# Optimization experiments

Measured on AMD Instinct MI355X. Metric: run time of the kernel, lower is better.

Reference implementation:

```python
import jax, jax.numpy as jnp
import numpy as np

B, S, D, H, DK = 2, 2048, 1024, 16, 64  # d_model = n_heads * d_k

def setup_inputs() -> dict:
    key = jax.random.key(0)
    ks = jax.random.split(key, 11)
    s = 1.0 / np.sqrt(D)
    return {
        "Q": jax.random.normal(ks[0], (B, S, D), jnp.float32),
        "K": jax.random.normal(ks[1], (B, S, D), jnp.float32),
        "V": jax.random.normal(ks[2], (B, S, D), jnp.float32),
        "wq": jax.random.normal(ks[3], (D, D), jnp.float32) * s,
        "bq": jnp.zeros((D,), jnp.float32),
        "wk": jax.random.normal(ks[4], (D, D), jnp.float32) * s,
        "bk": jnp.zeros((D,), jnp.float32),
        "wv": jax.random.normal(ks[5], (D, D), jnp.float32) * s,
        "bv": jnp.zeros((D,), jnp.float32),
        "wo": jax.random.normal(ks[6], (D, D), jnp.float32) * s,
        "bo": jnp.zeros((D,), jnp.float32),
    }

def reference(Q, K, V, wq, bq, wk, bk, wv, bv, wo, bo):
    # linear projections (torch Linear: x @ W^T + b)
    q = Q @ wq.T + bq
    k = K @ wk.T + bk
    v = V @ wv.T + bv
    # split heads -> [B, H, S, DK]
    def split(t):
        return t.reshape(B, S, H, DK).transpose(0, 2, 1, 3)
    q, k, v = split(q), split(k), split(v)
    scale = 1.0 / np.sqrt(DK)
    scores = jnp.einsum('bhqd,bhkd->bhqk', q, k) * scale  # [B,H,S,S]
    probs = jax.nn.softmax(scores, axis=-1)
    # dropout is identity in eval mode
    ctx = jnp.einsum('bhqk,bhkd->bhqd', probs, v)  # [B,H,S,DK]
    ctx = ctx.transpose(0, 2, 1, 3).reshape(B, S, D)
    return ctx @ wo.T + bo
```

## Files before the change

### kernel.cpp

```cpp
#include <hip/hip_runtime.h>

#define S_LEN 2048
#define DMODEL 1024
#define DHEAD 64

typedef _Float16 half8 __attribute__((ext_vector_type(8)));
typedef _Float16 half4 __attribute__((ext_vector_type(4)));
typedef float f32x4 __attribute__((ext_vector_type(4)));
typedef int i32x4 __attribute__((ext_vector_type(4)));

#define LOG2E 1.4426950408889634f

__device__ __forceinline__ void async_copy16(const void* g, void* l) {
  __builtin_amdgcn_global_load_lds((__attribute__((address_space(1))) const void*)g,
                                   (__attribute__((address_space(3))) void*)l,
                                   16, 0, 0);
}

#define WAIT_VMCNT(N) asm volatile("s_waitcnt vmcnt(" #N ")" ::: "memory")
#define WAIT_LGKM0() asm volatile("s_waitcnt lgkmcnt(0)" ::: "memory")
#define RAW_BARRIER() asm volatile("s_barrier" ::: "memory")

__global__ __launch_bounds__(256) void convert_w(const float* __restrict__ wq,
                                                 const float* __restrict__ wk,
                                                 const float* __restrict__ wv,
                                                 _Float16* __restrict__ dst) {
  const float* src = (blockIdx.y == 0) ? wq : (blockIdx.y == 1) ? wk : wv;
  _Float16* d = dst + (size_t)blockIdx.y * (DMODEL * DMODEL);
  int i = (blockIdx.x * 256 + threadIdx.x) * 4;
  float4 v = *(const float4*)(src + i);
  half4 h;
  h[0] = (_Float16)v.x; h[1] = (_Float16)v.y;
  h[2] = (_Float16)v.z; h[3] = (_Float16)v.w;
  *(half4*)(d + i) = h;
}

__global__ __launch_bounds__(256) void convert_wo(const float* __restrict__ wo,
                                                  _Float16* __restrict__ dst) {
  int i = (blockIdx.x * 256 + threadIdx.x) * 4;
  float4 v = *(const float4*)(wo + i);
  half4 h;
  h[0] = (_Float16)v.x; h[1] = (_Float16)v.y;
  h[2] = (_Float16)v.z; h[3] = (_Float16)v.w;
  *(half4*)(dst + i) = h;
}

__global__ __launch_bounds__(256, 3) void qkv_gemm(
    const float* __restrict__ Qf, const float* __restrict__ Kf, const float* __restrict__ Vf,
    const _Float16* __restrict__ wh,
    const float* __restrict__ bq, const float* __restrict__ bk, const float* __restrict__ bv,
    _Float16* __restrict__ qo, _Float16* __restrict__ ko, _Float16* __restrict__ vt) {
  __shared__ __align__(16) _Float16 Asb[3][128 * 32];
  __shared__ __align__(16) _Float16 Bsb[3][128 * 32];
  const int tid = threadIdx.x;
  const int wave = tid >> 6, lane = tid & 63;
  const int m15 = lane & 15, quad = lane >> 4;
  const int m0 = blockIdx.x * 128;
  const int y = blockIdx.y;
  const int sel = (y < 8) ? 2 : (y < 16) ? 0 : 1;
  const int n0 = (y & 7) * 128;
  const float* Ag = (sel == 0) ? Qf : (sel == 1) ? Kf : Vf;
  const _Float16* Wg = wh + (size_t)sel * (DMODEL * DMODEL);
  const float* bias = (sel == 0) ? bq : (sel == 1) ? bk : bv;

  const int wm = (wave & 1) * 64, wn = (wave >> 1) * 64;

  const int sr = tid >> 1, sc16 = (tid & 1) * 16;
  const int g0 = (tid & 1) * 2, asw = (sr >> 1) & 3;
  const int b_r = lane >> 2, b_g = (lane & 3) ^ ((lane >> 3) & 3);
  const int ra = ((quad ^ ((m15 >> 1) & 3)) << 4);

  f32x4 acc[4][4];
#pragma unroll
  for (int i = 0; i < 4; i++)
#pragma unroll
    for (int j = 0; j < 4; j++) {
      f32x4 z = {0.f, 0.f, 0.f, 0.f};
      acc[i][j] = z;
    }

  const float* ap = Ag + (size_t)(m0 + sr) * DMODEL + sc16;

  auto loadA = [&](int kk, float4 (&s)[4]) {
    const float* p = ap + kk;
    s[0] = ((const float4*)p)[0];
    s[1] = ((const float4*)p)[1];
    s[2] = ((const float4*)p)[2];
    s[3] = ((const float4*)p)[3];
  };
  auto writeA = [&](const float4 (&s)[4], int nb) {
    half8 h0, h1;
    h0[0] = (_Float16)s[0].x; h0[1] = (_Float16)s[0].y; h0[2] = (_Float16)s[0].z; h0[3] = (_Float16)s[0].w;
    h0[4] = (_Float16)s[1].x; h0[5] = (_Float16)s[1].y; h0[6] = (_Float16)s[1].z; h0[7] = (_Float16)s[1].w;
    h1[0] = (_Float16)s[2].x; h1[1] = (_Float16)s[2].y; h1[2] = (_Float16)s[2].z; h1[3] = (_Float16)s[2].w;
    h1[4] = (_Float16)s[3].x; h1[5] = (_Float16)s[3].y; h1[6] = (_Float16)s[3].z; h1[7] = (_Float16)s[3].w;
    char* rb = (char*)&Asb[nb][0] + sr * 64;
    *(half8*)(rb + ((g0 ^ asw) << 4)) = h0;
    *(half8*)(rb + (((g0 + 1) ^ asw) << 4)) = h1;
  };
  auto issueB = [&](int kk, int nb) {
#pragma unroll
    for (int p = 0; p < 2; p++) {
      int row = (p * 4 + wave) * 16 + b_r;
      async_copy16(Wg + (size_t)(n0 + row) * DMODEL + kk + b_g * 8,
                   (char*)&Bsb[nb][0] + p * 4096 + wave * 1024);
    }
  };
  auto compute = [&](int m3) {
    const char* ab = (const char*)&Asb[m3][0];
    const char* bb = (const char*)&Bsb[m3][0];
    half8 af[4], bf[4];
#pragma unroll
    for (int i = 0; i < 4; i++)
      af[i] = *(const half8*)(ab + (wm + i * 16 + m15) * 64 + ra);
#pragma unroll
    for (int j = 0; j < 4; j++)
      bf[j] = *(const half8*)(bb + (wn + j * 16 + m15) * 64 + ra);
#pragma unroll
    for (int i = 0; i < 4; i++)
#pragma unroll
      for (int j = 0; j < 4; j++)
        acc[i][j] = __builtin_amdgcn_mfma_f32_16x16x32_f16(af[i], bf[j], acc[i][j], 0, 0, 0);
  };

  float4 s0[4], s1[4], s2[4];

  issueB(0, 0);
  loadA(0, s0);
  issueB(32, 1);
  loadA(32, s1);
  loadA(64, s2);
  WAIT_VMCNT(10);
  writeA(s0, 0);
  WAIT_LGKM0();
  RAW_BARRIER();

  auto body = [&](int kt, int m3, int bB, int bW, float4 (&ld)[4], const float4 (&wr)[4],
                  int mode) {
    if (mode == 0) {
      issueB((kt + 2) * 32, bB);
      loadA((kt + 3) * 32, ld);
    } else if (mode == 1) {
      issueB((kt + 2) * 32, bB);
    }
    compute(m3);
    if (mode == 3) return;
    if (mode == 0) { WAIT_VMCNT(10); }
    else if (mode == 1) { WAIT_VMCNT(6); }
    else { WAIT_VMCNT(0); }
    writeA(wr, bW);
    WAIT_LGKM0();
    RAW_BARRIER();
  };

#pragma unroll 1
  for (int k3 = 0; k3 < 27; k3 += 3) {
    body(k3 + 0, 0, 2, 1, s0, s1, 0);
    body(k3 + 1, 1, 0, 2, s1, s2, 0);
    body(k3 + 2, 2, 1, 0, s2, s0, 0);
  }
  body(27, 0, 2, 1, s0, s1, 0);
  body(28, 1, 0, 2, s1, s2, 0);
  body(29, 2, 1, 0, s2, s0, 1);
  body(30, 0, 0, 1, s0, s1, 2);
  body(31, 1, 0, 0, s0, s0, 3);

  if (sel != 2) {
    _Float16* outp = (sel == 0) ? qo : ko;
    const float scale = (sel == 0) ? (0.125f * LOG2E) : 1.0f;
#pragma unroll
    for (int i = 0; i < 4; i++) {
#pragma unroll
      for (int j = 0; j < 4; j++) {
        int gn = n0 + wn + j * 16 + m15;
        float bb = bias[gn];
#pragma unroll
        for (int r = 0; r < 4; r++) {
          int gm = m0 + wm + i * 16 + quad * 4 + r;
          outp[(size_t)gm * DMODEL + gn] = (_Float16)((acc[i][j][r] + bb) * scale);
        }
      }
    }
  } else {
#pragma unroll
    for (int i = 0; i < 4; i++) {
      int gm0 = m0 + wm + i * 16 + quad * 4;
      int b = gm0 >> 11, s = gm0 & 2047;
#pragma unroll
      for (int j = 0; j < 4; j++) {
        int gn = n0 + wn + j * 16 + m15;
        int h = gn >> 6, dk = gn & 63;
        float bb = bias[gn];
        half4 hv;
        hv[0] = (_Float16)(acc[i][j][0] + bb);
        hv[1] = (_Float16)(acc[i][j][1] + bb);
        hv[2] = (_Float16)(acc[i][j][2] + bb);
        hv[3] = (_Float16)(acc[i][j][3] + bb);
        *(half4*)(vt + ((size_t)(b * 16 + h) * 64 + dk) * 2048 + s) = hv;
      }
    }
  }
}

__global__ __launch_bounds__(256) void attn_kernel(const _Float16* __restrict__ qh,
                                                   const _Float16* __restrict__ kh,
                                                   const _Float16* __restrict__ vt,
                                                   _Float16* __restrict__ ctx) {
  __shared__ __align__(16) char smem[49152];
  const int tid = threadIdx.x;
  const int wave = tid >> 6, lane = tid & 63;
  const int m15 = lane & 15, qd = lane >> 4;
  const int wq = wave >> 1, ws = wave & 1;
  const int q0 = blockIdx.x * 64;
  const int h = blockIdx.y, b = blockIdx.z;
  const size_t base = (size_t)b * S_LEN * DMODEL + (size_t)h * DHEAD;
  const size_t vbase = (size_t)(b * 16 + h) * 64 * 2048;

  half8 qf[2][2];
#pragma unroll
  for (int qt = 0; qt < 2; qt++) {
    const _Float16* qp = qh + base + (size_t)(q0 + wq * 32 + qt * 16 + m15) * DMODEL + qd * 8;
    qf[qt][0] = *(const half8*)qp;
    qf[qt][1] = *(const half8*)(qp + 32);
  }

  const int l8 = lane >> 3, s8 = lane & 7;
  const int swz = (s8 ^ l8) * 8;
  const _Float16* ksrc = kh + base + (size_t)(wave * 8 + l8) * DMODEL + swz;
  const _Float16* vsrc = vt + vbase + (size_t)(wave * 8 + l8) * S_LEN + swz;

  const int kgr = ((qd ^ (m15 & 7)) << 4);
  const int vgr = (((ws * 4 + qd) ^ (m15 & 7)) << 4);
  const int krow = ws * 32 + m15;

  auto stage = [&](int tile, int bufi) {
    const int kv = tile * 64;
    char* kd = smem + bufi * 8192 + wave * 1024;
    char* vd = smem + 24576 + bufi * 8192 + wave * 1024;
#pragma unroll
    for (int p = 0; p < 2; p++) {
      async_copy16(ksrc + (size_t)(kv + p * 32) * DMODEL, kd + p * 4096);
      async_copy16(vsrc + (size_t)(p * 32) * S_LEN + kv, vd + p * 4096);
    }
  };

  f32x4 acc[4][2];
#pragma unroll
  for (int i = 0; i < 4; i++)
#pragma unroll
    for (int j = 0; j < 2; j++) { f32x4 z = {0.f, 0.f, 0.f, 0.f}; acc[i][j] = z; }
  float ls[2] = {0.f, 0.f};

  stage(0, 0);
  stage(1, 1);
  WAIT_VMCNT(4);
  RAW_BARRIER();

  int bcur = 0, bnxt = 2;
  for (int it = 0; it < 32; it++) {
    if (it < 30) stage(it + 2, bnxt);
    const char* kb = smem + bcur * 8192;
    const char* vb = smem + 24576 + bcur * 8192;

    half8 kf[2][2];
#pragma unroll
    for (int t = 0; t < 2; t++) {
      kf[t][0] = *(const half8*)(kb + (krow + 16 * t) * 128 + kgr);
      kf[t][1] = *(const half8*)(kb + (krow + 16 * t) * 128 + (kgr ^ 64));
    }

    f32x4 sc[2][2];
#pragma unroll
    for (int t = 0; t < 2; t++)
#pragma unroll
      for (int qt = 0; qt < 2; qt++) {
        f32x4 z = {0.f, 0.f, 0.f, 0.f};
        sc[t][qt] = __builtin_amdgcn_mfma_f32_16x16x32_f16(kf[t][0], qf[qt][0], z, 0, 0, 0);
        sc[t][qt] = __builtin_amdgcn_mfma_f32_16x16x32_f16(kf[t][1], qf[qt][1], sc[t][qt], 0, 0, 0);
      }

    int pk[2][2][2];
#pragma unroll
    for (int t = 0; t < 2; t++)
#pragma unroll
      for (int qt = 0; qt < 2; qt++) {
        float e0 = __builtin_amdgcn_exp2f(sc[t][qt][0]);
        float e1 = __builtin_amdgcn_exp2f(sc[t][qt][1]);
        float e2 = __builtin_amdgcn_exp2f(sc[t][qt][2]);
        float e3 = __builtin_amdgcn_exp2f(sc[t][qt][3]);
        ls[qt] += (e0 + e1) + (e2 + e3);
        pk[t][qt][0] = __builtin_bit_cast(int, __builtin_amdgcn_cvt_pkrtz(e0, e1));
        pk[t][qt][1] = __builtin_bit_cast(int, __builtin_amdgcn_cvt_pkrtz(e2, e3));
      }

    half8 pA[2];
#pragma unroll
    for (int qt = 0; qt < 2; qt++) {
      i32x4 fh;
#pragma unroll
      for (int p = 0; p < 2; p++) {
        auto s1 = __builtin_amdgcn_permlane32_swap(pk[0][qt][p], pk[1][qt][p], false, false);
        auto s2 = __builtin_amdgcn_permlane16_swap(s1[0], s1[1], false, false);
        fh[p] = (int)s2[0];
        fh[2 + p] = (int)s2[1];
      }
      pA[qt] = __builtin_bit_cast(half8, fh);
    }

#pragma unroll
    for (int td = 0; td < 4; td++) {
      half8 vf = *(const half8*)(vb + (td * 16 + m15) * 128 + vgr);
#pragma unroll
      for (int qt = 0; qt < 2; qt++)
        acc[td][qt] = __builtin_amdgcn_mfma_f32_16x16x32_f16(vf, pA[qt], acc[td][qt], 0, 0, 0);
    }
    if (it < 30) { WAIT_VMCNT(4); } else { WAIT_VMCNT(0); }
    RAW_BARRIER();
    bcur = (bcur == 2) ? 0 : bcur + 1;
    bnxt = (bnxt == 2) ? 0 : bnxt + 1;
  }

  float* Ored = (float*)smem;
  float* Lred = (float*)(smem + 17408);

#pragma unroll
  for (int qt = 0; qt < 2; qt++) {
    ls[qt] += __shfl_xor(ls[qt], 16);
    ls[qt] += __shfl_xor(ls[qt], 32);
  }

  if (ws == 1) {
#pragma unroll
    for (int qt = 0; qt < 2; qt++) {
      int q = wq * 32 + qt * 16 + m15;
      if (qd == 0) Lred[q] = ls[qt];
#pragma unroll
      for (int td = 0; td < 4; td++)
        *(f32x4*)&Ored[q * 68 + td * 16 + qd * 4] = acc[td][qt];
    }
  }
  __syncthreads();

  if (ws == 0) {
#pragma unroll
    for (int qt = 0; qt < 2; qt++) {
      int q = wq * 32 + qt * 16 + m15;
      const float inv = 1.0f / (ls[qt] + Lred[q]);
#pragma unroll
      for (int td = 0; td < 4; td++) {
        f32x4 o = acc[td][qt] + *(const f32x4*)&Ored[q * 68 + td * 16 + qd * 4];
        half4 hv;
#pragma unroll
        for (int r = 0; r < 4; r++) hv[r] = (_Float16)(o[r] * inv);
        *(half4*)(ctx + base + (size_t)(q0 + q) * DMODEL + td * 16 + qd * 4) = hv;
      }
    }
  }
}

__global__ __launch_bounds__(256, 4) void out_gemm(const _Float16* __restrict__ ch,
                                                   const _Float16* __restrict__ who,
                                                   const float* __restrict__ bo,
                                                   float* __restrict__ out) {
  __shared__ __align__(16) _Float16 As[3][64 * 32];
  __shared__ __align__(16) _Float16 Bs[3][128 * 32];
  const int tid = threadIdx.x;
  const int wave = tid >> 6, lane = tid & 63;
  const int m15 = lane & 15, quad = lane >> 4;
  const int m0 = blockIdx.x * 64, n0 = blockIdx.y * 128;
  const int wm = (wave & 1) * 32, wn = (wave >> 1) * 64;
  const int b_r = lane >> 2, b_g = (lane & 3) ^ ((lane >> 3) & 3);
  const int rgr = ((quad ^ ((m15 >> 1) & 3)) << 4);

  f32x4 acc[2][4];
#pragma unroll
  for (int i = 0; i < 2; i++)
#pragma unroll
    for (int j = 0; j < 4; j++) {
      f32x4 z = {0.f, 0.f, 0.f, 0.f};
      acc[i][j] = z;
    }

  auto issueTile = [&](int kk, int nb) {
    {
      int row = wave * 16 + b_r;
      async_copy16(ch + (size_t)(m0 + row) * DMODEL + kk + b_g * 8,
                   (char*)&As[nb][0] + wave * 1024);
    }
#pragma unroll
    for (int p = 0; p < 2; p++) {
      int row = (p * 4 + wave) * 16 + b_r;
      async_copy16(who + (size_t)(n0 + row) * DMODEL + kk + b_g * 8,
                   (char*)&Bs[nb][0] + p * 4096 + wave * 1024);
    }
  };
  auto compute = [&](int m3) {
    half8 af[2], bf[4];
#pragma unroll
    for (int i = 0; i < 2; i++)
      af[i] = *(const half8*)((char*)&As[m3][0] + (wm + i * 16 + m15) * 64 + rgr);
#pragma unroll
    for (int j = 0; j < 4; j++)
      bf[j] = *(const half8*)((char*)&Bs[m3][0] + (wn + j * 16 + m15) * 64 + rgr);
#pragma unroll
    for (int i = 0; i < 2; i++)
#pragma unroll
      for (int j = 0; j < 4; j++)
        acc[i][j] = __builtin_amdgcn_mfma_f32_16x16x32_f16(af[i], bf[j], acc[i][j], 0, 0, 0);
  };

  issueTile(0, 0);
  issueTile(32, 1);
  WAIT_VMCNT(3);
  RAW_BARRIER();

#pragma unroll 1
  for (int k3 = 0; k3 < 30; k3 += 3) {
    issueTile((k3 + 2) * 32, 2); compute(0); WAIT_VMCNT(3); RAW_BARRIER();
    issueTile((k3 + 3) * 32, 0); compute(1); WAIT_VMCNT(3); RAW_BARRIER();
    issueTile((k3 + 4) * 32, 1); compute(2); WAIT_VMCNT(3); RAW_BARRIER();
  }
  compute(0);
  WAIT_VMCNT(0);
  RAW_BARRIER();
  compute(1);

#pragma unroll
  for (int i = 0; i < 2; i++) {
#pragma unroll
    for (int j = 0; j < 4; j++) {
      int gn = n0 + wn + j * 16 + m15;
      float bb = bo[gn];
#pragma unroll
      for (int r = 0; r < 4; r++) {
        int gm = m0 + wm + i * 16 + quad * 4 + r;
        out[(size_t)gm * DMODEL + gn] = acc[i][j][r] + bb;
      }
    }
  }
}

extern "C" void kernel_launch(void* const* d_in, const int* in_sizes, int n_in,
                              void* d_out, int out_size, void* d_ws, size_t ws_size,
                              hipStream_t stream) {
  (void)in_sizes; (void)n_in; (void)out_size; (void)ws_size;
  const float* Q  = (const float*)d_in[0];
  const float* K  = (const float*)d_in[1];
  const float* V  = (const float*)d_in[2];
  const float* wq = (const float*)d_in[3];
  const float* bq = (const float*)d_in[4];
  const float* wk = (const float*)d_in[5];
  const float* bk = (const float*)d_in[6];
  const float* wv = (const float*)d_in[7];
  const float* bv = (const float*)d_in[8];
  const float* wo = (const float*)d_in[9];
  const float* bo = (const float*)d_in[10];
  float* out = (float*)d_out;

  _Float16* qh = (_Float16*)d_out;
  _Float16* kh = qh + (size_t)4194304;
  _Float16* vt = (_Float16*)d_ws;
  _Float16* wh = vt + (size_t)4194304;
  _Float16* ch = vt + (size_t)4194304;
  _Float16* who = (_Float16*)d_ws;

  convert_w<<<dim3(1024, 3), 256, 0, stream>>>(wq, wk, wv, wh);
  qkv_gemm<<<dim3(32, 24), 256, 0, stream>>>(Q, K, V, wh, bq, bk, bv, qh, kh, vt);
  attn_kernel<<<dim3(32, 16, 2), 256, 0, stream>>>(qh, kh, vt, ch);
  convert_wo<<<dim3(1024), 256, 0, stream>>>(wo, who);
  out_gemm<<<dim3(64, 8), 256, 0, stream>>>(ch, who, bo, out);
}
```

Measured before the change: 232.0 us.

## Load V fragments directly from global in attention, restructure output GEMM tiling

The attention kernel stops staging V through LDS and reads the V^T fragments straight from global memory into registers each iteration. K staging drops from triple to double buffering, with __syncthreads replacing the explicit vmcnt waits, and the reduction scratch padding shrinks so total LDS is about 16KB instead of 48KB, which may raise occupancy. The output GEMM moves to 64x64 tiles with a 64-wide K step and double buffering, doubling the grid. The risk is that uncoalesced, unshared V global loads now sit in the critical path of each iteration, and the full barrier may serialize the K prefetch.

```diff
diff --git a/kernel.cpp b/kernel.cpp
--- a/kernel.cpp
+++ b/kernel.cpp
@@ -206,7 +206,7 @@
                                                    const _Float16* __restrict__ kh,
                                                    const _Float16* __restrict__ vt,
                                                    _Float16* __restrict__ ctx) {
-  __shared__ __align__(16) char smem[49152];
+  __shared__ __align__(16) char smem[16640];
   const int tid = threadIdx.x;
   const int wave = tid >> 6, lane = tid & 63;
   const int m15 = lane & 15, qd = lane >> 4;
@@ -227,22 +227,11 @@
   const int l8 = lane >> 3, s8 = lane & 7;
   const int swz = (s8 ^ l8) * 8;
   const _Float16* ksrc = kh + base + (size_t)(wave * 8 + l8) * DMODEL + swz;
-  const _Float16* vsrc = vt + vbase + (size_t)(wave * 8 + l8) * S_LEN + swz;
+  char* kdst = smem + wave * 1024;
 
   const int kgr = ((qd ^ (m15 & 7)) << 4);
-  const int vgr = (((ws * 4 + qd) ^ (m15 & 7)) << 4);
   const int krow = ws * 32 + m15;
-
-  auto stage = [&](int tile, int bufi) {
-    const int kv = tile * 64;
-    char* kd = smem + bufi * 8192 + wave * 1024;
-    char* vd = smem + 24576 + bufi * 8192 + wave * 1024;
-#pragma unroll
-    for (int p = 0; p < 2; p++) {
-      async_copy16(ksrc + (size_t)(kv + p * 32) * DMODEL, kd + p * 4096);
-      async_copy16(vsrc + (size_t)(p * 32) * S_LEN + kv, vd + p * 4096);
-    }
-  };
+  const _Float16* vrow = vt + vbase + (size_t)m15 * 2048 + ws * 32 + qd * 8;
 
   f32x4 acc[4][2];
 #pragma unroll
@@ -251,16 +240,21 @@
     for (int j = 0; j < 2; j++) { f32x4 z = {0.f, 0.f, 0.f, 0.f}; acc[i][j] = z; }
   float ls[2] = {0.f, 0.f};
 
-  stage(0, 0);
-  stage(1, 1);
-  WAIT_VMCNT(4);
-  RAW_BARRIER();
-
-  int bcur = 0, bnxt = 2;
+#pragma unroll
+  for (int p = 0; p < 2; p++)
+    async_copy16(ksrc + (size_t)(p * 32) * DMODEL, kdst + p * 4096);
+  __syncthreads();
+
   for (int it = 0; it < 32; it++) {
-    if (it < 30) stage(it + 2, bnxt);
-    const char* kb = smem + bcur * 8192;
-    const char* vb = smem + 24576 + bcur * 8192;
+    const int buf = it & 1;
+    if (it < 31) {
+      const int kv = (it + 1) * 64;
+#pragma unroll
+      for (int p = 0; p < 2; p++)
+        async_copy16(ksrc + (size_t)(kv + p * 32) * DMODEL, kdst + (buf ^ 1) * 8192 + p * 4096);
+    }
+    const char* kb = smem + buf * 8192;
+    const int kv0 = it * 64;
 
     half8 kf[2][2];
 #pragma unroll
@@ -278,6 +272,11 @@
         sc[t][qt] = __builtin_amdgcn_mfma_f32_16x16x32_f16(kf[t][0], qf[qt][0], z, 0, 0, 0);
         sc[t][qt] = __builtin_amdgcn_mfma_f32_16x16x32_f16(kf[t][1], qf[qt][1], sc[t][qt], 0, 0, 0);
       }
+
+    half8 vf0 = *(const half8*)(vrow + kv0);
+    half8 vf1 = *(const half8*)(vrow + 16 * 2048 + kv0);
+    half8 vf2 = *(const half8*)(vrow + 32 * 2048 + kv0);
+    half8 vf3 = *(const half8*)(vrow + 48 * 2048 + kv0);
 
     int pk[2][2][2];
 #pragma unroll
@@ -308,20 +307,17 @@
     }
 
 #pragma unroll
-    for (int td = 0; td < 4; td++) {
-      half8 vf = *(const half8*)(vb + (td * 16 + m15) * 128 + vgr);
-#pragma unroll
-      for (int qt = 0; qt < 2; qt++)
-        acc[td][qt] = __builtin_amdgcn_mfma_f32_16x16x32_f16(vf, pA[qt], acc[td][qt], 0, 0, 0);
-    }
-    if (it < 30) { WAIT_VMCNT(4); } else { WAIT_VMCNT(0); }
-    RAW_BARRIER();
-    bcur = (bcur == 2) ? 0 : bcur + 1;
-    bnxt = (bnxt == 2) ? 0 : bnxt + 1;
+    for (int qt = 0; qt < 2; qt++) {
+      acc[0][qt] = __builtin_amdgcn_mfma_f32_16x16x32_f16(vf0, pA[qt], acc[0][qt], 0, 0, 0);
+      acc[1][qt] = __builtin_amdgcn_mfma_f32_16x16x32_f16(vf1, pA[qt], acc[1][qt], 0, 0, 0);
+      acc[2][qt] = __builtin_amdgcn_mfma_f32_16x16x32_f16(vf2, pA[qt], acc[2][qt], 0, 0, 0);
+      acc[3][qt] = __builtin_amdgcn_mfma_f32_16x16x32_f16(vf3, pA[qt], acc[3][qt], 0, 0, 0);
+    }
+    __syncthreads();
   }
 
   float* Ored = (float*)smem;
-  float* Lred = (float*)(smem + 17408);
+  float* Lred = (float*)(smem + 16384);
 
 #pragma unroll
   for (int qt = 0; qt < 2; qt++) {
@@ -336,7 +332,7 @@
       if (qd == 0) Lred[q] = ls[qt];
 #pragma unroll
       for (int td = 0; td < 4; td++)
-        *(f32x4*)&Ored[q * 68 + td * 16 + qd * 4] = acc[td][qt];
+        *(f32x4*)&Ored[q * 64 + td * 16 + qd * 4] = acc[td][qt];
     }
   }
   __syncthreads();
@@ -348,7 +344,7 @@
       const float inv = 1.0f / (ls[qt] + Lred[q]);
 #pragma unroll
       for (int td = 0; td < 4; td++) {
-        f32x4 o = acc[td][qt] + *(const f32x4*)&Ored[q * 68 + td * 16 + qd * 4];
+        f32x4 o = acc[td][qt] + *(const f32x4*)&Ored[q * 64 + td * 16 + qd * 4];
         half4 hv;
 #pragma unroll
         for (int r = 0; r < 4; r++) hv[r] = (_Float16)(o[r] * inv);
@@ -358,77 +354,76 @@
   }
 }
 
-__global__ __launch_bounds__(256, 4) void out_gemm(const _Float16* __restrict__ ch,
-                                                   const _Float16* __restrict__ who,
-                                                   const float* __restrict__ bo,
-                                                   float* __restrict__ out) {
-  __shared__ __align__(16) _Float16 As[3][64 * 32];
-  __shared__ __align__(16) _Float16 Bs[3][128 * 32];
+__global__ __launch_bounds__(256) void out_gemm(const _Float16* __restrict__ ch,
+                                                const _Float16* __restrict__ who,
+                                                const float* __restrict__ bo,
+                                                float* __restrict__ out) {
+  __shared__ __align__(16) _Float16 As[2][64 * 64];
+  __shared__ __align__(16) _Float16 Bs[2][64 * 64];
   const int tid = threadIdx.x;
   const int wave = tid >> 6, lane = tid & 63;
   const int m15 = lane & 15, quad = lane >> 4;
-  const int m0 = blockIdx.x * 64, n0 = blockIdx.y * 128;
-  const int wm = (wave & 1) * 32, wn = (wave >> 1) * 64;
-  const int b_r = lane >> 2, b_g = (lane & 3) ^ ((lane >> 3) & 3);
-  const int rgr = ((quad ^ ((m15 >> 1) & 3)) << 4);
-
-  f32x4 acc[2][4];
+  const int m0 = blockIdx.x * 64, n0 = blockIdx.y * 64;
+  const int wm = (wave & 1) * 32, wn = (wave >> 1) * 32;
+
+  const int l8 = lane >> 3, s8 = lane & 7;
+  const int swz = (s8 ^ l8) * 8;
+  const _Float16* asrc = ch + (size_t)(m0 + wave * 8 + l8) * DMODEL + swz;
+  const _Float16* bsrc = who + (size_t)(n0 + wave * 8 + l8) * DMODEL + swz;
+  char* adst = (char*)&As[0][0] + wave * 1024;
+  char* bdst = (char*)&Bs[0][0] + wave * 1024;
+
+  const int rg0 = ((quad ^ (m15 & 7)) << 4);
+
+  f32x4 acc[2][2];
 #pragma unroll
   for (int i = 0; i < 2; i++)
 #pragma unroll
-    for (int j = 0; j < 4; j++) {
+    for (int j = 0; j < 2; j++) {
       f32x4 z = {0.f, 0.f, 0.f, 0.f};
       acc[i][j] = z;
     }
 
-  auto issueTile = [&](int kk, int nb) {
-    {
-      int row = wave * 16 + b_r;
-      async_copy16(ch + (size_t)(m0 + row) * DMODEL + kk + b_g * 8,
-                   (char*)&As[nb][0] + wave * 1024);
-    }
+  auto stage = [&](int kk, int bufi) {
 #pragma unroll
     for (int p = 0; p < 2; p++) {
-      int row = (p * 4 + wave) * 16 + b_r;
-      async_copy16(who + (size_t)(n0 + row) * DMODEL + kk + b_g * 8,
-                   (char*)&Bs[nb][0] + p * 4096 + wave * 1024);
-    }
-  };
-  auto compute = [&](int m3) {
-    half8 af[2], bf[4];
+      async_copy16(asrc + (size_t)(p * 32) * DMODEL + kk, adst + bufi * 8192 + p * 4096);
+      async_copy16(bsrc + (size_t)(p * 32) * DMODEL + kk, bdst + bufi * 8192 + p * 4096);
+    }
+  };
+
+  stage(0, 0);
+  __syncthreads();
+
+  for (int kt = 0; kt < 16; kt++) {
+    const int buf = kt & 1;
+    if (kt < 15) stage((kt + 1) * 64, buf ^ 1);
+    const char* ab = (const char*)&As[buf][0];
+    const char* bb = (const char*)&Bs[buf][0];
+    half8 af[2][2], bf[2][2];
+#pragma unroll
+    for (int i = 0; i < 2; i++) {
+      af[i][0] = *(const half8*)(ab + (wm + i * 16 + m15) * 128 + rg0);
+      af[i][1] = *(const half8*)(ab + (wm + i * 16 + m15) * 128 + (rg0 ^ 64));
+    }
+#pragma unroll
+    for (int j = 0; j < 2; j++) {
+      bf[j][0] = *(const half8*)(bb + (wn + j * 16 + m15) * 128 + rg0);
+      bf[j][1] = *(const half8*)(bb + (wn + j * 16 + m15) * 128 + (rg0 ^ 64));
+    }
 #pragma unroll
     for (int i = 0; i < 2; i++)
-      af[i] = *(const half8*)((char*)&As[m3][0] + (wm + i * 16 + m15) * 64 + rgr);
-#pragma unroll
-    for (int j = 0; j < 4; j++)
-      bf[j] = *(const half8*)((char*)&Bs[m3][0] + (wn + j * 16 + m15) * 64 + rgr);
-#pragma unroll
-    for (int i = 0; i < 2; i++)
-#pragma unroll
-      for (int j = 0; j < 4; j++)
-        acc[i][j] = __builtin_amdgcn_mfma_f32_16x16x32_f16(af[i], bf[j], acc[i][j], 0, 0, 0);
-  };
-
-  issueTile(0, 0);
-  issueTile(32, 1);
-  WAIT_VMCNT(3);
-  RAW_BARRIER();
-
-#pragma unroll 1
-  for (int k3 = 0; k3 < 30; k3 += 3) {
-    issueTile((k3 + 2) * 32, 2); compute(0); WAIT_VMCNT(3); RAW_BARRIER();
-    issueTile((k3 + 3) * 32, 0); compute(1); WAIT_VMCNT(3); RAW_BARRIER();
-    issueTile((k3 + 4) * 32, 1); compute(2); WAIT_VMCNT(3); RAW_BARRIER();
-  }
-  compute(0);
-  WAIT_VMCNT(0);
-  RAW_BARRIER();
-  compute(1);
-
+#pragma unroll
+      for (int j = 0; j < 2; j++) {
+        acc[i][j] = __builtin_amdgcn_mfma_f32_16x16x32_f16(af[i][0], bf[j][0], acc[i][j], 0, 0, 0);
+        acc[i][j] = __builtin_amdgcn_mfma_f32_16x16x32_f16(af[i][1], bf[j][1], acc[i][j], 0, 0, 0);
+      }
+    __syncthreads();
+  }
 #pragma unroll
   for (int i = 0; i < 2; i++) {
 #pragma unroll
-    for (int j = 0; j < 4; j++) {
+    for (int j = 0; j < 2; j++) {
       int gn = n0 + wn + j * 16 + m15;
       float bb = bo[gn];
 #pragma unroll
@@ -468,5 +463,5 @@
   qkv_gemm<<<dim3(32, 24), 256, 0, stream>>>(Q, K, V, wh, bq, bk, bv, qh, kh, vt);
   attn_kernel<<<dim3(32, 16, 2), 256, 0, stream>>>(qh, kh, vt, ch);
   convert_wo<<<dim3(1024), 256, 0, stream>>>(wo, who);
-  out_gemm<<<dim3(64, 8), 256, 0, stream>>>(ch, who, bo, out);
-}
+  out_gemm<<<dim3(64, 16), 256, 0, stream>>>(ch, who, bo, out);
+}
```

After: 261.8 us. 1.13x slower.
